# Kernel optimization log

Measured on AMD Instinct MI355X. Metric: run time of the kernel, lower is better.

Reference implementation:

```python
import jax, jax.numpy as jnp
import numpy as np

N = 100000
E = 1600000
IN_C, HID_C, OUT_C = 128, 64, 16


def setup_inputs() -> dict:
    key = jax.random.key(0)
    k1, k2, k3, k4, k5 = jax.random.split(key, 5)
    x = jax.random.normal(k1, (N, IN_C), dtype=jnp.float32)
    edge_index = jax.random.randint(k2, (2, E), 0, N, dtype=jnp.int64)
    edge_weight = jax.random.uniform(k3, (E,), dtype=jnp.float32)
    # GCNConv weights (Glorot init, bias=False)
    W1 = jax.random.normal(k4, (IN_C, HID_C), dtype=jnp.float32) * (1.0 / np.sqrt(IN_C))
    W2 = jax.random.normal(k5, (HID_C, OUT_C), dtype=jnp.float32) * (1.0 / np.sqrt(HID_C))
    return {"x": x, "edge_index": edge_index, "edge_weight": edge_weight, "W1": W1, "W2": W2}


def _gcn_norm(edge_index, edge_weight, num_nodes):
    # add self loops with weight 1 (PyG gcn_norm with add_self_loops=True)
    loop = jnp.arange(num_nodes, dtype=edge_index.dtype)
    row = jnp.concatenate([edge_index[0], loop])
    col = jnpp_concat = jnp.concatenate([edge_index[1], loop])
    w = jnp.concatenate([edge_weight, jnp.ones((num_nodes,), edge_weight.dtype)])
    deg = jax.ops.segment_sum(w, col, num_segments=num_nodes)
    dinv = jnp.where(deg > 0, jax.lax.rsqrt(deg), 0.0)
    norm = dinv[row] * w * dinv[col]
    return row, col, norm


def _gcn_conv(x, W, row, col, norm, num_nodes):
    h = x @ W                              # [N, C_out] dense projection
    msg = h[row] * norm[:, None]           # gather + scale per edge
    return jax.ops.segment_sum(msg, col, num_segments=num_nodes)  # scatter-add at dst


def reference(x, edge_index, edge_weight, W1, W2):
    num_nodes = x.shape[0]
    row, col, norm = _gcn_norm(edge_index, edge_weight, num_nodes)
    h = _gcn_conv(x, W1, row, col, norm, num_nodes)
    h = jax.nn.relu(h)  # dropout_rate == 0 / eval -> identity
    h = _gcn_conv(h, W2, row, col, norm, num_nodes)
    return jax.nn.log_softmax(h, axis=1)
```

## Files before the change

### kernel.cpp

```cpp
#include <hip/hip_runtime.h>
#include <hip/hip_fp16.h>
#include <math.h>

constexpr int IN_C = 128, HID_C = 64, OUT_C = 16;
constexpr int BSH = 7;
constexpr int BCAP = 2560;
constexpr int REC_PT = BCAP / 256;
constexpr int TILE = 4096;
constexpr float WSC = 33554432.0f;
constexpr float WINV15 = 1.0f / 32768.0f;

using f16x8 = __attribute__((ext_vector_type(8))) _Float16;
using f16x4 = __attribute__((ext_vector_type(4))) _Float16;
using f32x4 = __attribute__((ext_vector_type(4))) float;

__global__ __launch_bounds__(256) void k_hist(const int* __restrict__ col, int* __restrict__ histG,
                                              int E, int nb) {
  __shared__ int h[1024];
  int t = threadIdx.x, tile = blockIdx.x;
  for (int i = t; i < nb; i += 256) h[i] = 0;
  __syncthreads();
  int base = tile * TILE;
#pragma unroll
  for (int u = 0; u < TILE / 256; ++u) {
    int e = base + u * 256 + t;
    if (e < E) atomicAdd(&h[col[e] >> BSH], 1);
  }
  __syncthreads();
  for (int i = t; i < nb; i += 256) histG[(size_t)tile * nb + i] = h[i];
}

__global__ __launch_bounds__(256) void k_cscan(int* __restrict__ histG, int* __restrict__ btot,
                                               int T, int nb) {
  int b = blockIdx.x, t = threadIdx.x;
  __shared__ int s[512];
  int i0 = t, i1 = t + 256;
  s[i0] = (i0 < T) ? histG[(size_t)i0 * nb + b] : 0;
  s[i1] = (i1 < T) ? histG[(size_t)i1 * nb + b] : 0;
  __syncthreads();
  int c0 = s[i0], c1 = s[i1];
  for (int off = 1; off < 512; off <<= 1) {
    int a0 = (i0 >= off) ? s[i0 - off] : 0;
    int a1 = (i1 >= off) ? s[i1 - off] : 0;
    __syncthreads();
    s[i0] += a0; s[i1] += a1;
    __syncthreads();
  }
  if (i0 < T) histG[(size_t)i0 * nb + b] = s[i0] - c0;
  if (i1 < T) histG[(size_t)i1 * nb + b] = s[i1] - c1;
  if (t == 0) btot[b] = s[511];
}

__global__ __launch_bounds__(256) void k_scat2(const int* __restrict__ row, const int* __restrict__ col,
                                               const float* __restrict__ w, const int* __restrict__ histG,
                                               uint2* __restrict__ rec, int E, int nb) {
  __shared__ int soff[1024];
  int t = threadIdx.x, tile = blockIdx.x;
  for (int i = t; i < nb; i += 256) soff[i] = histG[(size_t)tile * nb + i];
  __syncthreads();
  int base = tile * TILE;
#pragma unroll
  for (int u = 0; u < TILE / 256; ++u) {
    int e = base + u * 256 + t;
    if (e < E) {
      int r = row[e], d = col[e];
      int b = d >> BSH;
      unsigned lo = (unsigned)(d & ((1 << BSH) - 1));
      unsigned wf = __float2uint_rn(w[e] * WSC);
      if (wf > 33554431u) wf = 33554431u;
      int slot = atomicAdd(&soff[b], 1);
      if (slot < BCAP)
        rec[(size_t)b * BCAP + slot] = make_uint2((unsigned)r, (lo << 25) | wf);
    }
  }
}

__global__ __launch_bounds__(256) void k_buck(const int* __restrict__ btot, const uint2* __restrict__ rec,
                                              unsigned* __restrict__ pairs, int* __restrict__ ptrg,
                                              int* __restrict__ cntg, float* __restrict__ dinvg,
                                              int n) {
  int b = blockIdx.x;
  int t = threadIdx.x;
  int cnt = btot[b];
  if (cnt > BCAP) cnt = BCAP;
  __shared__ int lcnt[128];
  __shared__ float lws[128];
  __shared__ int lptr[128];
  __shared__ unsigned sp[BCAP];
  if (t < 128) { lcnt[t] = 0; lws[t] = 0.f; }
  __syncthreads();
  uint2 rv[REC_PT];
  int rk[REC_PT];
#pragma unroll
  for (int u = 0; u < REC_PT; ++u) {
    int i = u * 256 + t;
    if (i < cnt) {
      uint2 v = rec[(size_t)b * BCAP + i];
      rv[u] = v;
      int lo = v.y >> 25;
      rk[u] = atomicAdd(&lcnt[lo], 1);
      atomicAdd(&lws[lo], (float)(v.y & 0x1FFFFFFu) * (1.0f / WSC));
    }
  }
  __syncthreads();
  if (t < 128) lptr[t] = lcnt[t];
  __syncthreads();
  for (int off = 1; off < 128; off <<= 1) {
    int v = (t < 128 && t >= off) ? lptr[t - off] : 0;
    __syncthreads();
    if (t < 128 && t >= off) lptr[t] += v;
    __syncthreads();
  }
  if (t < 128) {
    int d = (b << BSH) + t;
    if (d < n) {
      ptrg[d] = b * BCAP + lptr[t] - lcnt[t];
      cntg[d] = lcnt[t];
      dinvg[d] = rsqrtf(1.0f + lws[t]);
    }
  }
#pragma unroll
  for (int u = 0; u < REC_PT; ++u) {
    int i = u * 256 + t;
    if (i < cnt) {
      uint2 v = rv[u];
      int lo = v.y >> 25;
      unsigned wq = ((v.y & 0x1FFFFFFu) + 512u) >> 10;
      if (wq > 32767u) wq = 32767u;
      sp[(lptr[lo] - lcnt[lo]) + rk[u]] = (v.x << 15) | wq;
    }
  }
  __syncthreads();
  for (int i = t; i < cnt; i += 256)
    pairs[(size_t)b * BCAP + i] = sp[i];
}

__global__ __launch_bounds__(256) void k_gemm1(const float* __restrict__ x, const float* __restrict__ W1,
                                               const float* __restrict__ dinv,
                                               __half* __restrict__ h1h, int n) {
  __shared__ _Float16 w1t[HID_C][IN_C];
  int t = threadIdx.x;
  for (int i = t; i < IN_C * HID_C / 4; i += 256) {
    float4 v = ((const float4*)W1)[i];
    int k = (i * 4) / HID_C;
    int c = (i * 4) % HID_C;
    w1t[c + 0][k] = (_Float16)v.x;
    w1t[c + 1][k] = (_Float16)v.y;
    w1t[c + 2][k] = (_Float16)v.z;
    w1t[c + 3][k] = (_Float16)v.w;
  }
  __syncthreads();
  int wave = t >> 6, lane = t & 63;
  int row0 = (blockIdx.x * 4 + wave) * 16;
  if (row0 >= n) return;
  int lrow = lane & 15, lkg = lane >> 4;
  bool rvalid = (row0 + lrow) < n;
  const float* xr = x + (size_t)(row0 + lrow) * IN_C;
  f32x4 acc[4];
#pragma unroll
  for (int cg = 0; cg < 4; ++cg) acc[cg] = (f32x4){0.f, 0.f, 0.f, 0.f};
#pragma unroll
  for (int ks = 0; ks < 4; ++ks) {
    int k0 = ks * 32 + lkg * 8;
    f16x8 a;
    if (rvalid) {
      float4 u0 = *(const float4*)&xr[k0];
      float4 u1 = *(const float4*)&xr[k0 + 4];
      a[0] = (_Float16)u0.x; a[1] = (_Float16)u0.y; a[2] = (_Float16)u0.z; a[3] = (_Float16)u0.w;
      a[4] = (_Float16)u1.x; a[5] = (_Float16)u1.y; a[6] = (_Float16)u1.z; a[7] = (_Float16)u1.w;
    } else {
#pragma unroll
      for (int j = 0; j < 8; ++j) a[j] = (_Float16)0.f;
    }
#pragma unroll
    for (int cg = 0; cg < 4; ++cg) {
      f16x8 bfrag = *(const f16x8*)&w1t[cg * 16 + lrow][k0];
      acc[cg] = __builtin_amdgcn_mfma_f32_16x16x32_f16(a, bfrag, acc[cg], 0, 0, 0);
    }
  }
  float dv[4];
#pragma unroll
  for (int r = 0; r < 4; ++r) {
    int gr = row0 + lkg * 4 + r;
    dv[r] = (gr < n) ? dinv[gr] : 0.f;
  }
#pragma unroll
  for (int cg = 0; cg < 4; ++cg) {
#pragma unroll
    for (int r = 0; r < 4; ++r) {
      int gr = row0 + lkg * 4 + r;
      if (gr < n)
        h1h[(size_t)gr * HID_C + cg * 16 + lrow] = __float2half_rn(dv[r] * acc[cg][r]);
    }
  }
}

__global__ __launch_bounds__(256) void k_agg1f(const int* __restrict__ ptr, const int* __restrict__ cnt,
                                               const unsigned* __restrict__ pairs, const float* __restrict__ dinv,
                                               const __half* __restrict__ h1h, const float* __restrict__ W2,
                                               __half* __restrict__ h2h, int n) {
  __shared__ float w2s[HID_C * OUT_C];
  __shared__ __align__(16) float s[4][68];
  int t = threadIdx.x;
  ((float4*)w2s)[t] = ((const float4*)W2)[t];
  __syncthreads();
  int wv = t >> 6, lane = t & 63;
  int g = lane >> 4;
  int c4 = (lane & 15) * 4;
  int d = blockIdx.x * 4 + wv;
  if (d < n) {
    d = __builtin_amdgcn_readfirstlane(d);
    int k = ptr[d], end = k + cnt[d];
    float dd = dinv[d];
    f32x4 acc = {0.f, 0.f, 0.f, 0.f};
    if (g == 0) {
      f16x4 sv = *(const f16x4*)&h1h[(size_t)d * HID_C + c4];
      acc[0] = (float)sv[0]; acc[1] = (float)sv[1];
      acc[2] = (float)sv[2]; acc[3] = (float)sv[3];
    }
    int last = end - 1;
    for (; k < end; k += 32) {
      unsigned p[8]; float w[8]; f16x4 v[8];
#pragma unroll
      for (int u = 0; u < 8; ++u) {
        int idx = k + u * 4 + g;
        int ic = (idx <= last) ? idx : last;
        p[u] = pairs[ic];
        w[u] = (idx <= last) ? (float)(p[u] & 32767u) * WINV15 : 0.f;
      }
#pragma unroll
      for (int u = 0; u < 8; ++u)
        v[u] = *(const f16x4*)&h1h[(size_t)(p[u] >> 15) * HID_C + c4];
#pragma unroll
      for (int u = 0; u < 8; ++u) {
        acc[0] = fmaf(w[u], (float)v[u][0], acc[0]);
        acc[1] = fmaf(w[u], (float)v[u][1], acc[1]);
        acc[2] = fmaf(w[u], (float)v[u][2], acc[2]);
        acc[3] = fmaf(w[u], (float)v[u][3], acc[3]);
      }
    }
#pragma unroll
    for (int i = 0; i < 4; ++i) {
      acc[i] += __shfl_xor(acc[i], 16);
      acc[i] += __shfl_xor(acc[i], 32);
    }
    if (g == 0) {
      float4 r;
      r.x = fmaxf(dd * acc[0], 0.f);
      r.y = fmaxf(dd * acc[1], 0.f);
      r.z = fmaxf(dd * acc[2], 0.f);
      r.w = fmaxf(dd * acc[3], 0.f);
      *(float4*)&s[wv][c4] = r;
    }
  } else {
    if (g == 0) *(float4*)&s[wv][c4] = make_float4(0.f, 0.f, 0.f, 0.f);
  }
  __syncthreads();
  if (t < 64) {
    int nl = t >> 4, j = t & 15;
    int dn = blockIdx.x * 4 + nl;
    if (dn < n) {
      float a2 = 0.f;
#pragma unroll
      for (int c = 0; c < HID_C; ++c) a2 = fmaf(s[nl][c], w2s[c * OUT_C + j], a2);
      h2h[(size_t)dn * OUT_C + j] = __float2half_rn(dinv[dn] * a2);
    }
  }
}

__global__ __launch_bounds__(256) void k_agg2(const int* __restrict__ ptr, const int* __restrict__ cnt,
                                              const unsigned* __restrict__ pairs, const float* __restrict__ dinv,
                                              const __half* __restrict__ h2h, float* __restrict__ out, int n) {
  int t = threadIdx.x;
  int d = blockIdx.x * 16 + (t >> 4);
  if (d >= n) return;
  int j = t & 15;
  int k = ptr[d], end = k + cnt[d];
  float dd = dinv[d];
  float acc = __half2float(h2h[(size_t)d * OUT_C + j]);
  for (; k + 8 <= end; k += 8) {
    unsigned p[8];
    float v[8];
#pragma unroll
    for (int u = 0; u < 8; ++u) p[u] = pairs[k + u];
#pragma unroll
    for (int u = 0; u < 8; ++u)
      v[u] = __half2float(h2h[(size_t)(p[u] >> 15) * OUT_C + j]);
#pragma unroll
    for (int u = 0; u < 8; ++u) acc = fmaf((float)(p[u] & 32767u) * WINV15, v[u], acc);
  }
  if (k + 4 <= end) {
    unsigned p[4];
    float v[4];
#pragma unroll
    for (int u = 0; u < 4; ++u) p[u] = pairs[k + u];
#pragma unroll
    for (int u = 0; u < 4; ++u)
      v[u] = __half2float(h2h[(size_t)(p[u] >> 15) * OUT_C + j]);
#pragma unroll
    for (int u = 0; u < 4; ++u) acc = fmaf((float)(p[u] & 32767u) * WINV15, v[u], acc);
    k += 4;
  }
  for (; k < end; ++k) {
    unsigned p = pairs[k];
    acc = fmaf((float)(p & 32767u) * WINV15, __half2float(h2h[(size_t)(p >> 15) * OUT_C + j]), acc);
  }
  float lg = dd * acc;
  float mx = lg;
#pragma unroll
  for (int off = 8; off; off >>= 1) mx = fmaxf(mx, __shfl_xor(mx, off, 16));
  float sm = expf(lg - mx);
#pragma unroll
  for (int off = 8; off; off >>= 1) sm += __shfl_xor(sm, off, 16);
  out[(size_t)d * OUT_C + j] = lg - mx - logf(sm);
}

extern "C" void kernel_launch(void* const* d_in, const int* in_sizes, int n_in,
                              void* d_out, int out_size, void* d_ws, size_t ws_size,
                              hipStream_t stream) {
  const float* x  = (const float*)d_in[0];
  const int*   ei = (const int*)d_in[1];
  const float* ew = (const float*)d_in[2];
  const float* W1 = (const float*)d_in[3];
  const float* W2 = (const float*)d_in[4];
  const int N = in_sizes[0] / IN_C;
  const int E = in_sizes[2];
  const int* row = ei;
  const int* col = ei + E;
  float* out = (float*)d_out;
  const int NBUK = (N + (1 << BSH) - 1) >> BSH;
  const int T = (E + TILE - 1) / TILE;

  char* p = (char*)d_ws;
  unsigned* pairs = (unsigned*)p;     p += (size_t)NBUK * BCAP * 4;
  int*   ptr  = (int*)p;              p += (size_t)N * 4;
  int*   cnt  = (int*)p;              p += (size_t)N * 4;
  float* dinv = (float*)p;            p += (size_t)N * 4;
  int*   histG= (int*)p;              p += (size_t)T * NBUK * 4;
  int*   btot = (int*)p;              p += (size_t)NBUK * 4;
  char*  uni  = p;                    p += (size_t)N * HID_C * 4;
  uint2* rec  = (uint2*)uni;
  __half* h1h = (__half*)uni;
  __half* h2h = (__half*)(uni + (size_t)N * HID_C * 2);

  dim3 b(256);
  k_hist <<<T, b, 0, stream>>>(col, histG, E, NBUK);
  k_cscan<<<NBUK, b, 0, stream>>>(histG, btot, T, NBUK);
  k_scat2<<<T, b, 0, stream>>>(row, col, ew, histG, rec, E, NBUK);
  k_buck <<<NBUK, b, 0, stream>>>(btot, rec, pairs, ptr, cnt, dinv, N);
  k_gemm1<<<(N + 63) / 64, b, 0, stream>>>(x, W1, dinv, h1h, N);
  k_agg1f<<<(N + 3) / 4, b, 0, stream>>>(ptr, cnt, pairs, dinv, h1h, W2, h2h, N);
  k_agg2 <<<(N + 15) / 16, b, 0, stream>>>(ptr, cnt, pairs, dinv, h2h, out, N);
}
```

Baseline: 149.7 us.

## Fuse edge histogram and scatter into per-tile local sort, scan in bucket kernel

```diff
diff --git a/kernel.cpp b/kernel.cpp
--- a/kernel.cpp
+++ b/kernel.cpp
@@ -14,51 +14,40 @@
 using f16x4 = __attribute__((ext_vector_type(4))) _Float16;
 using f32x4 = __attribute__((ext_vector_type(4))) float;
 
-__global__ __launch_bounds__(256) void k_hist(const int* __restrict__ col, int* __restrict__ histG,
-                                              int E, int nb) {
-  __shared__ int h[1024];
+__global__ __launch_bounds__(256) void k_tile(const int* __restrict__ row, const int* __restrict__ col,
+                                              const float* __restrict__ w, int* __restrict__ histG,
+                                              uint2* __restrict__ rec, int E, int nb) {
+  __shared__ int hcnt[1024];
+  __shared__ int hoff[1024];
+  __shared__ int cs[256];
   int t = threadIdx.x, tile = blockIdx.x;
-  for (int i = t; i < nb; i += 256) h[i] = 0;
+  for (int i = t; i < 1024; i += 256) hcnt[i] = 0;
   __syncthreads();
   int base = tile * TILE;
 #pragma unroll
   for (int u = 0; u < TILE / 256; ++u) {
     int e = base + u * 256 + t;
-    if (e < E) atomicAdd(&h[col[e] >> BSH], 1);
-  }
-  __syncthreads();
-  for (int i = t; i < nb; i += 256) histG[(size_t)tile * nb + i] = h[i];
-}
-
-__global__ __launch_bounds__(256) void k_cscan(int* __restrict__ histG, int* __restrict__ btot,
-                                               int T, int nb) {
-  int b = blockIdx.x, t = threadIdx.x;
-  __shared__ int s[512];
-  int i0 = t, i1 = t + 256;
-  s[i0] = (i0 < T) ? histG[(size_t)i0 * nb + b] : 0;
-  s[i1] = (i1 < T) ? histG[(size_t)i1 * nb + b] : 0;
-  __syncthreads();
-  int c0 = s[i0], c1 = s[i1];
-  for (int off = 1; off < 512; off <<= 1) {
-    int a0 = (i0 >= off) ? s[i0 - off] : 0;
-    int a1 = (i1 >= off) ? s[i1 - off] : 0;
-    __syncthreads();
-    s[i0] += a0; s[i1] += a1;
-    __syncthreads();
-  }
-  if (i0 < T) histG[(size_t)i0 * nb + b] = s[i0] - c0;
-  if (i1 < T) histG[(size_t)i1 * nb + b] = s[i1] - c1;
-  if (t == 0) btot[b] = s[511];
-}
-
-__global__ __launch_bounds__(256) void k_scat2(const int* __restrict__ row, const int* __restrict__ col,
-                                               const float* __restrict__ w, const int* __restrict__ histG,
-                                               uint2* __restrict__ rec, int E, int nb) {
-  __shared__ int soff[1024];
-  int t = threadIdx.x, tile = blockIdx.x;
-  for (int i = t; i < nb; i += 256) soff[i] = histG[(size_t)tile * nb + i];
-  __syncthreads();
-  int base = tile * TILE;
+    if (e < E) atomicAdd(&hcnt[col[e] >> BSH], 1);
+  }
+  __syncthreads();
+  int c0 = hcnt[4 * t] + hcnt[4 * t + 1] + hcnt[4 * t + 2] + hcnt[4 * t + 3];
+  cs[t] = c0;
+  __syncthreads();
+  for (int off = 1; off < 256; off <<= 1) {
+    int v = (t >= off) ? cs[t - off] : 0;
+    __syncthreads();
+    cs[t] += v;
+    __syncthreads();
+  }
+  int r0 = cs[t] - c0;
+  hoff[4 * t] = r0; r0 += hcnt[4 * t];
+  hoff[4 * t + 1] = r0; r0 += hcnt[4 * t + 1];
+  hoff[4 * t + 2] = r0; r0 += hcnt[4 * t + 2];
+  hoff[4 * t + 3] = r0;
+  __syncthreads();
+  for (int i = t; i < nb; i += 256)
+    histG[(size_t)tile * nb + i] = (hoff[i] << 13) | hcnt[i];
+  __syncthreads();
 #pragma unroll
   for (int u = 0; u < TILE / 256; ++u) {
     int e = base + u * 256 + t;
@@ -68,34 +57,50 @@
       unsigned lo = (unsigned)(d & ((1 << BSH) - 1));
       unsigned wf = __float2uint_rn(w[e] * WSC);
       if (wf > 33554431u) wf = 33554431u;
-      int slot = atomicAdd(&soff[b], 1);
-      if (slot < BCAP)
-        rec[(size_t)b * BCAP + slot] = make_uint2((unsigned)r, (lo << 25) | wf);
-    }
-  }
-}
-
-__global__ __launch_bounds__(256) void k_buck(const int* __restrict__ btot, const uint2* __restrict__ rec,
-                                              unsigned* __restrict__ pairs, int* __restrict__ ptrg,
-                                              int* __restrict__ cntg, float* __restrict__ dinvg,
-                                              int n) {
-  int b = blockIdx.x;
-  int t = threadIdx.x;
-  int cnt = btot[b];
-  if (cnt > BCAP) cnt = BCAP;
+      int slot = atomicAdd(&hoff[b], 1);
+      rec[(size_t)tile * TILE + slot] = make_uint2((unsigned)r, (lo << 25) | wf);
+    }
+  }
+}
+
+__global__ __launch_bounds__(256) void k_buck2(const int* __restrict__ histG, const uint2* __restrict__ rec,
+                                               unsigned* __restrict__ pairs, int* __restrict__ ptrg,
+                                               int* __restrict__ cntg, float* __restrict__ dinvg,
+                                               int n, int T, int nb) {
+  int b = blockIdx.x, t = threadIdx.x;
+  __shared__ int s[512];
+  __shared__ int off_s[512];
   __shared__ int lcnt[128];
   __shared__ float lws[128];
   __shared__ int lptr[128];
   __shared__ unsigned sp[BCAP];
+  int i0 = t, i1 = t + 256;
+  int v0 = (i0 < T) ? histG[(size_t)i0 * nb + b] : 0;
+  int v1 = (i1 < T) ? histG[(size_t)i1 * nb + b] : 0;
+  off_s[i0] = v0 >> 13; off_s[i1] = v1 >> 13;
+  s[i0] = v0 & 8191; s[i1] = v1 & 8191;
   if (t < 128) { lcnt[t] = 0; lws[t] = 0.f; }
   __syncthreads();
+  for (int off = 1; off < 512; off <<= 1) {
+    int a0 = (i0 >= off) ? s[i0 - off] : 0;
+    int a1 = (i1 >= off) ? s[i1 - off] : 0;
+    __syncthreads();
+    s[i0] += a0; s[i1] += a1;
+    __syncthreads();
+  }
+  int cnt = s[511];
+  if (cnt > BCAP) cnt = BCAP;
   uint2 rv[REC_PT];
   int rk[REC_PT];
 #pragma unroll
   for (int u = 0; u < REC_PT; ++u) {
     int i = u * 256 + t;
     if (i < cnt) {
-      uint2 v = rec[(size_t)b * BCAP + i];
+      int lo_ = 0, hi_ = 511;
+      while (lo_ < hi_) { int m = (lo_ + hi_) >> 1; if (s[m] > i) hi_ = m; else lo_ = m + 1; }
+      int seg = lo_;
+      int ex = seg ? s[seg - 1] : 0;
+      uint2 v = rec[(size_t)seg * TILE + off_s[seg] + (i - ex)];
       rv[u] = v;
       int lo = v.y >> 25;
       rk[u] = atomicAdd(&lcnt[lo], 1);
@@ -337,17 +342,14 @@
   int*   cnt  = (int*)p;              p += (size_t)N * 4;
   float* dinv = (float*)p;            p += (size_t)N * 4;
   int*   histG= (int*)p;              p += (size_t)T * NBUK * 4;
-  int*   btot = (int*)p;              p += (size_t)NBUK * 4;
   char*  uni  = p;                    p += (size_t)N * HID_C * 4;
   uint2* rec  = (uint2*)uni;
   __half* h1h = (__half*)uni;
   __half* h2h = (__half*)(uni + (size_t)N * HID_C * 2);
 
   dim3 b(256);
-  k_hist <<<T, b, 0, stream>>>(col, histG, E, NBUK);
-  k_cscan<<<NBUK, b, 0, stream>>>(histG, btot, T, NBUK);
-  k_scat2<<<T, b, 0, stream>>>(row, col, ew, histG, rec, E, NBUK);
-  k_buck <<<NBUK, b, 0, stream>>>(btot, rec, pairs, ptr, cnt, dinv, N);
+  k_tile <<<T, b, 0, stream>>>(row, col, ew, histG, rec, E, NBUK);
+  k_buck2<<<NBUK, b, 0, stream>>>(histG, rec, pairs, ptr, cnt, dinv, N, T, NBUK);
   k_gemm1<<<(N + 63) / 64, b, 0, stream>>>(x, W1, dinv, h1h, N);
   k_agg1f<<<(N + 3) / 4, b, 0, stream>>>(ptr, cnt, pairs, dinv, h1h, W2, h2h, N);
   k_agg2 <<<(N + 15) / 16, b, 0, stream>>>(ptr, cnt, pairs, dinv, h2h, out, N);
```

Result: faster. 142.7 us (-4.7%).
